# Kernel optimization log

Hardware: AMD Instinct MI355X
Metric: run time of the kernel (lower is better)

Reference implementation:

```python
import jax, jax.numpy as jnp
import numpy as np
from jax import lax

B, T, I, H, O = 128, 512, 256, 512, 256


def setup_inputs() -> dict:
    key = jax.random.key(0)
    ks = jax.random.split(key, 7)
    s_ih = 1.0 / np.sqrt(H)
    return {
        "inputs": jax.random.normal(ks[0], (B, T, I), dtype=jnp.float32),
        "W_ih": jax.random.uniform(ks[1], (H, I), jnp.float32, -s_ih, s_ih),
        "b_ih": jax.random.uniform(ks[2], (H,), jnp.float32, -s_ih, s_ih),
        "W_hh": jax.random.uniform(ks[3], (H, H), jnp.float32, -s_ih, s_ih),
        "b_hh": jax.random.uniform(ks[4], (H,), jnp.float32, -s_ih, s_ih),
        "W_out": jax.random.uniform(ks[5], (O, H), jnp.float32, -s_ih, s_ih),
        "b_out": jax.random.uniform(ks[6], (O,), jnp.float32, -s_ih, s_ih),
        "h0": jnp.zeros((H,), dtype=jnp.float32),
    }


def reference(inputs, W_ih, b_ih, W_hh, b_hh, W_out, b_out, h0):
    # inputs: [B, T, I]; returns readout of last hidden state: [B, O]
    Bsz, Tlen = inputs.shape[0], inputs.shape[1]
    inv_T = jnp.asarray(1.0 / Tlen, dtype=inputs.dtype)
    # Precompute input projection for all timesteps (one big GEMM):
    # x_proj[b,t,h] = inputs @ W_ih.T + b_ih + b_hh
    x_proj = jnp.einsum('bti,hi->bth', inputs, W_ih) + (b_ih + b_hh)
    x_proj_t = jnp.swapaxes(x_proj, 0, 1)  # [T, B, H]

    def step(h, xp):
        # RNNCell: tanh(xp + h @ W_hh.T); residual scaling by 1/T
        h_new = jnp.tanh(xp + h @ W_hh.T) * inv_T + h
        return h_new, None

    h_init = jnp.broadcast_to(h0, (Bsz, h0.shape[0]))
    h_last, _ = lax.scan(step, h_init, x_proj_t)
    return h_last @ W_out.T + b_out
```

## Files before the change

kernel.cpp:

```cpp
#include <hip/hip_runtime.h>
#include <stdint.h>

#define NB 128
#define NT 512
#define NI 256
#define NH 512
#define NO 256

__device__ __forceinline__ uint16_t f2bf(float x) {
  uint32_t u = __float_as_uint(x);
  return (uint16_t)((u + 0x7fffu + ((u >> 16) & 1u)) >> 16);
}
__device__ __forceinline__ uint32_t pack2bf(float a, float b) {
  return (uint32_t)f2bf(a) | ((uint32_t)f2bf(b) << 16);
}

__device__ __forceinline__ float fast_tanh(float x) {
  float e = __expf(2.0f * x);
#if __has_builtin(__builtin_amdgcn_rcpf)
  return 1.0f - 2.0f * __builtin_amdgcn_rcpf(e + 1.0f);
#else
  return 1.0f - 2.0f / (e + 1.0f);
#endif
}

typedef __bf16 bf16x8 __attribute__((ext_vector_type(8)));
typedef float f32x4 __attribute__((ext_vector_type(4)));

__device__ __forceinline__ f32x4 mfma16(bf16x8 a, uint4 b, f32x4 c) {
  return __builtin_amdgcn_mfma_f32_16x16x32_bf16(a, __builtin_bit_cast(bf16x8, b), c, 0, 0, 0);
}

__global__ __launch_bounds__(256) void prep_kernel(const float* __restrict__ Whh,
                                                   const float* __restrict__ Wih,
                                                   const float* __restrict__ Wout,
                                                   const float* __restrict__ bih,
                                                   const float* __restrict__ bhh,
                                                   uint4* __restrict__ WB,
                                                   float* __restrict__ WoT,
                                                   uint4* __restrict__ WihF,
                                                   float* __restrict__ BS) {
  int idx = blockIdx.x * 256 + threadIdx.x;
  if (idx < 32768) {
    int q = idx >> 9, t = idx & 511;
    int u = q >> 4, tk = q & 15;
    int n = (t >> 6) * 64 + u * 16 + (t & 15);
    int kb = tk * 32 + ((t >> 4) & 3) * 8;
    const float* row = Whh + (size_t)n * NH + kb;
    float4 f0 = *(const float4*)row;
    float4 f1 = *(const float4*)(row + 4);
    uint4 wq;
    wq.x = pack2bf(f0.x, f0.y);
    wq.y = pack2bf(f0.z, f0.w);
    wq.z = pack2bf(f1.x, f1.y);
    wq.w = pack2bf(f1.z, f1.w);
    WB[idx] = wq;
  } else if (idx < 49152) {
    int i = idx - 32768;
    int l = i & 63;
    int uk = i >> 6;
    int k0 = uk & 7, u = uk >> 3;
    int n = u * 16 + (l & 15);
    int kb = k0 * 32 + (l >> 4) * 8;
    const float* row = Wih + (size_t)n * NI + kb;
    float4 f0 = *(const float4*)row;
    float4 f1 = *(const float4*)(row + 4);
    uint4 wq;
    wq.x = pack2bf(f0.x, f0.y);
    wq.y = pack2bf(f0.z, f0.w);
    wq.z = pack2bf(f1.x, f1.y);
    wq.w = pack2bf(f1.z, f1.w);
    WihF[i] = wq;
  } else if (idx < 81920) {
    int i = idx - 49152;
    int o4 = (i & 63) * 4;
    int k = i >> 6;
    float4 v;
    v.x = Wout[(size_t)(o4 + 0) * NH + k];
    v.y = Wout[(size_t)(o4 + 1) * NH + k];
    v.z = Wout[(size_t)(o4 + 2) * NH + k];
    v.w = Wout[(size_t)(o4 + 3) * NH + k];
    *(float4*)&WoT[(size_t)k * NO + o4] = v;
  } else if (idx < 82432) {
    int n = idx - 81920;
    BS[n] = bih[n] + bhh[n];
  }
}

__global__ __launch_bounds__(256, 2) void xproj_kernel(const float* __restrict__ A,
                                                       const uint4* __restrict__ WihF,
                                                       const float* __restrict__ BS,
                                                       uint16_t* __restrict__ XP) {
  const int w = threadIdx.x >> 6;
  const int l = threadIdx.x & 63;
  const int sl = l & 15, quad = l >> 4;
  const int m = blockIdx.x * 64 + w * 16 + sl;

  f32x4 acc[32] = {};
  const float* arow = A + (size_t)m * NI;

  for (int k0 = 0; k0 < 8; ++k0) {
    float4 f0 = *(const float4*)(arow + k0 * 32 + quad * 8);
    float4 f1 = *(const float4*)(arow + k0 * 32 + quad * 8 + 4);
    uint4 ap;
    ap.x = pack2bf(f0.x, f0.y);
    ap.y = pack2bf(f0.z, f0.w);
    ap.z = pack2bf(f1.x, f1.y);
    ap.w = pack2bf(f1.z, f1.w);
    bf16x8 afrag = __builtin_bit_cast(bf16x8, ap);
#pragma unroll
    for (int u = 0; u < 32; ++u) {
      uint4 bp = WihF[(u * 8 + k0) * 64 + l];
      acc[u] = __builtin_amdgcn_mfma_f32_16x16x32_bf16(
          __builtin_bit_cast(bf16x8, bp), afrag, acc[u], 0, 0, 0);
    }
  }

  uint16_t* xrow = XP + (size_t)m * NH;
#pragma unroll
  for (int u = 0; u < 32; ++u) {
    float4 bs = *(const float4*)(BS + u * 16 + quad * 4);
    uint2 pw;
    pw.x = pack2bf(acc[u][0] + bs.x, acc[u][1] + bs.y);
    pw.y = pack2bf(acc[u][2] + bs.z, acc[u][3] + bs.w);
    *(uint2*)(xrow + u * 16 + quad * 4) = pw;
  }
}

__global__ __launch_bounds__(512, 2) void recur_kernel(const uint4* __restrict__ WB,
                                                       const float* __restrict__ WoT,
                                                       const uint16_t* __restrict__ XP,
                                                       const float* __restrict__ h0,
                                                       const float* __restrict__ bout,
                                                       float* __restrict__ out) {
  __shared__ uint4 WL[12][512];
  __shared__ __align__(16) uint16_t h2[2][NH];
  __shared__ float hsf[NH];
  const int t = threadIdx.x;
  const int b = blockIdx.x;
  const int w = t >> 6;
  const int sl = t & 15, quad = (t >> 4) & 3;
  const int myn = w * 64 + quad * 16 + sl;
  const float invT = 1.0f / (float)NT;

  uint4 Wr[52];
#pragma unroll
  for (int q = 0; q < 52; ++q) Wr[q] = WB[q * 512 + t];
#pragma unroll
  for (int i = 0; i < 12; ++i) WL[i][t] = WB[(52 + i) * 512 + t];

  float hj = h0[myn];
  h2[0][myn] = f2bf(hj);
  __syncthreads();

  const uint16_t* xpb = XP + (size_t)b * NT * NH + myn;

  for (int ts = 0; ts < NT; ++ts) {
    const int cur = ts & 1;
    float xpj = __uint_as_float((uint32_t)xpb[(size_t)ts * NH] << 16);

    const uint16_t* hbuf = h2[cur];
    f32x4 acc0 = {}, acc1 = {}, acc2 = {}, acc3 = {};
#pragma unroll
    for (int tk = 0; tk < 16; ++tk) {
      bf16x8 hfrag = *(const bf16x8*)(hbuf + tk * 32 + quad * 8);
      acc0 = mfma16(hfrag, Wr[tk], acc0);
      acc1 = mfma16(hfrag, Wr[16 + tk], acc1);
      acc2 = mfma16(hfrag, Wr[32 + tk], acc2);
      uint4 w3 = (tk < 4) ? Wr[48 + tk] : WL[tk - 4][t];
      acc3 = mfma16(hfrag, w3, acc3);
    }
    float y = (quad == 0) ? acc0[0] : (quad == 1) ? acc1[0] : (quad == 2) ? acc2[0] : acc3[0];
    float hnew = fmaf(fast_tanh(xpj + y), invT, hj);
    hj = hnew;
    h2[cur ^ 1][myn] = f2bf(hnew);
    __syncthreads();
  }

  hsf[myn] = hj;
  __syncthreads();

  if (t < NO) {
    float c0 = 0.f, c1 = 0.f;
#pragma unroll 4
    for (int k = 0; k < NH; k += 2) {
      c0 = fmaf(WoT[(size_t)k * NO + t], hsf[k], c0);
      c1 = fmaf(WoT[(size_t)(k + 1) * NO + t], hsf[k + 1], c1);
    }
    out[(size_t)b * NO + t] = c0 + c1 + bout[t];
  }
}

extern "C" void kernel_launch(void* const* d_in, const int* in_sizes, int n_in,
                              void* d_out, int out_size, void* d_ws, size_t ws_size,
                              hipStream_t stream) {
  const float* inputs = (const float*)d_in[0];
  const float* Wih    = (const float*)d_in[1];
  const float* bih    = (const float*)d_in[2];
  const float* Whh    = (const float*)d_in[3];
  const float* bhh    = (const float*)d_in[4];
  const float* Wout   = (const float*)d_in[5];
  const float* bout   = (const float*)d_in[6];
  const float* h0     = (const float*)d_in[7];
  float* out = (float*)d_out;

  char* ws = (char*)d_ws;
  uint4*    WB   = (uint4*)ws;
  float*    WoT  = (float*)(ws + (512u << 10));
  uint4*    WihF = (uint4*)(ws + (1024u << 10));
  float*    BS   = (float*)(ws + (1280u << 10));
  uint16_t* XP   = (uint16_t*)(ws + (1536u << 10));

  hipLaunchKernelGGL(prep_kernel, dim3(322), dim3(256), 0, stream,
                     Whh, Wih, Wout, bih, bhh, WB, WoT, WihF, BS);
  hipLaunchKernelGGL(xproj_kernel, dim3(NB * NT / 64), dim3(256), 0, stream,
                     inputs, WihF, BS, XP);
  hipLaunchKernelGGL(recur_kernel, dim3(NB), dim3(512), 0, stream,
                     WB, WoT, XP, h0, bout, out);
}
```

Measured before the change: 943.2 us.

## Retile input projection GEMM with register-resident weight slices and double-buffered A loads

The xproj kernel previously had each wave hold all 512 output columns for one 16-row tile and reload W_ih fragments from global memory for every MFMA. Now a 2D grid splits the N dimension into 8 groups of 64 columns. Each wave keeps its 32-fragment W_ih slice in registers, loops over 4 row tiles, and double-buffers the loading and bf16 packing of A rows to overlap them with the MFMAs. In exchange, the fp32 input rows are read 8 times, once per column group, instead of once, and register pressure from the resident weights remains.

```diff
diff --git a/kernel.cpp b/kernel.cpp
--- a/kernel.cpp
+++ b/kernel.cpp
@@ -29,6 +29,9 @@
 
 __device__ __forceinline__ f32x4 mfma16(bf16x8 a, uint4 b, f32x4 c) {
   return __builtin_amdgcn_mfma_f32_16x16x32_bf16(a, __builtin_bit_cast(bf16x8, b), c, 0, 0, 0);
+}
+__device__ __forceinline__ f32x4 mfma16_ab(uint4 a, bf16x8 b, f32x4 c) {
+  return __builtin_amdgcn_mfma_f32_16x16x32_bf16(__builtin_bit_cast(bf16x8, a), b, c, 0, 0, 0);
 }
 
 __global__ __launch_bounds__(256) void prep_kernel(const float* __restrict__ Whh,
@@ -87,6 +90,42 @@
   }
 }
 
+__device__ __forceinline__ void ld_pack(uint4 (&af)[8], const float* __restrict__ A,
+                                        int mt, int sl, int quad) {
+  const float* ar = A + (size_t)(mt * 16 + sl) * NI + quad * 8;
+#pragma unroll
+  for (int k0 = 0; k0 < 8; ++k0) {
+    float4 f0 = *(const float4*)(ar + k0 * 32);
+    float4 f1 = *(const float4*)(ar + k0 * 32 + 4);
+    uint4 ap;
+    ap.x = pack2bf(f0.x, f0.y);
+    ap.y = pack2bf(f0.z, f0.w);
+    ap.z = pack2bf(f1.x, f1.y);
+    ap.w = pack2bf(f1.z, f1.w);
+    af[k0] = ap;
+  }
+}
+
+__device__ __forceinline__ void do_tile(const uint4 (&af)[8], const uint4 (&Wb)[32],
+                                        const float4 (&bs)[4], uint16_t* __restrict__ XP,
+                                        int g, int mt, int sl, int quad) {
+  f32x4 acc[4] = {};
+#pragma unroll
+  for (int k0 = 0; k0 < 8; ++k0) {
+    bf16x8 a = __builtin_bit_cast(bf16x8, af[k0]);
+#pragma unroll
+    for (int u = 0; u < 4; ++u) acc[u] = mfma16_ab(Wb[u * 8 + k0], a, acc[u]);
+  }
+  uint16_t* xrow = XP + (size_t)(mt * 16 + sl) * NH + g * 64 + quad * 4;
+#pragma unroll
+  for (int u = 0; u < 4; ++u) {
+    uint2 pw;
+    pw.x = pack2bf(acc[u][0] + bs[u].x, acc[u][1] + bs[u].y);
+    pw.y = pack2bf(acc[u][2] + bs[u].z, acc[u][3] + bs[u].w);
+    *(uint2*)(xrow + u * 16) = pw;
+  }
+}
+
 __global__ __launch_bounds__(256, 2) void xproj_kernel(const float* __restrict__ A,
                                                        const uint4* __restrict__ WihF,
                                                        const float* __restrict__ BS,
@@ -94,37 +133,29 @@
   const int w = threadIdx.x >> 6;
   const int l = threadIdx.x & 63;
   const int sl = l & 15, quad = l >> 4;
-  const int m = blockIdx.x * 64 + w * 16 + sl;
-
-  f32x4 acc[32] = {};
-  const float* arow = A + (size_t)m * NI;
-
-  for (int k0 = 0; k0 < 8; ++k0) {
-    float4 f0 = *(const float4*)(arow + k0 * 32 + quad * 8);
-    float4 f1 = *(const float4*)(arow + k0 * 32 + quad * 8 + 4);
-    uint4 ap;
-    ap.x = pack2bf(f0.x, f0.y);
-    ap.y = pack2bf(f0.z, f0.w);
-    ap.z = pack2bf(f1.x, f1.y);
-    ap.w = pack2bf(f1.z, f1.w);
-    bf16x8 afrag = __builtin_bit_cast(bf16x8, ap);
-#pragma unroll
-    for (int u = 0; u < 32; ++u) {
-      uint4 bp = WihF[(u * 8 + k0) * 64 + l];
-      acc[u] = __builtin_amdgcn_mfma_f32_16x16x32_bf16(
-          __builtin_bit_cast(bf16x8, bp), afrag, acc[u], 0, 0, 0);
-    }
-  }
-
-  uint16_t* xrow = XP + (size_t)m * NH;
-#pragma unroll
-  for (int u = 0; u < 32; ++u) {
-    float4 bs = *(const float4*)(BS + u * 16 + quad * 4);
-    uint2 pw;
-    pw.x = pack2bf(acc[u][0] + bs.x, acc[u][1] + bs.y);
-    pw.y = pack2bf(acc[u][2] + bs.z, acc[u][3] + bs.w);
-    *(uint2*)(xrow + u * 16 + quad * 4) = pw;
-  }
+  const int g = blockIdx.y;
+  const int mt0 = blockIdx.x * 16 + w * 4;
+
+  uint4 Wb[32];
+#pragma unroll
+  for (int u = 0; u < 4; ++u)
+#pragma unroll
+    for (int k0 = 0; k0 < 8; ++k0)
+      Wb[u * 8 + k0] = WihF[(size_t)((g * 4 + u) * 8 + k0) * 64 + l];
+
+  float4 bs[4];
+#pragma unroll
+  for (int u = 0; u < 4; ++u) bs[u] = *(const float4*)(BS + (g * 4 + u) * 16 + quad * 4);
+
+  uint4 afA[8], afB[8];
+  ld_pack(afA, A, mt0 + 0, sl, quad);
+  ld_pack(afB, A, mt0 + 1, sl, quad);
+  do_tile(afA, Wb, bs, XP, g, mt0 + 0, sl, quad);
+  ld_pack(afA, A, mt0 + 2, sl, quad);
+  do_tile(afB, Wb, bs, XP, g, mt0 + 1, sl, quad);
+  ld_pack(afB, A, mt0 + 3, sl, quad);
+  do_tile(afA, Wb, bs, XP, g, mt0 + 2, sl, quad);
+  do_tile(afB, Wb, bs, XP, g, mt0 + 3, sl, quad);
 }
 
 __global__ __launch_bounds__(512, 2) void recur_kernel(const uint4* __restrict__ WB,
@@ -213,7 +244,7 @@
 
   hipLaunchKernelGGL(prep_kernel, dim3(322), dim3(256), 0, stream,
                      Whh, Wih, Wout, bih, bhh, WB, WoT, WihF, BS);
-  hipLaunchKernelGGL(xproj_kernel, dim3(NB * NT / 64), dim3(256), 0, stream,
+  hipLaunchKernelGGL(xproj_kernel, dim3(NB * NT / 256, 8), dim3(256), 0, stream,
                      inputs, WihF, BS, XP);
   hipLaunchKernelGGL(recur_kernel, dim3(NB), dim3(512), 0, stream,
                      WB, WoT, XP, h0, bout, out);
```

Measured after the change: 929.9 us. Within noise of the previous version (-1.4%).

## Keep W_ih fragments in registers in xproj and stage A tiles via LDS

Applied to the files above, without the earlier changes.

The input-projection kernel now has each wave hold its 128-column slice of W_ih in registers for the whole block. Each block loops over 16 row tiles, converting input rows to bf16 into double-buffered shared memory. This removes the repeated global loads of W_ih for every 64-row tile and reuses the weights across 256 rows, at the cost of 64 uint4 registers per thread and fewer blocks. The recurrence kernel also keeps all 64 W_hh fragments in registers instead of spilling 12 into LDS, which raises register pressure and risks spills or lower occupancy.

```diff
diff --git a/kernel.cpp b/kernel.cpp
--- a/kernel.cpp
+++ b/kernel.cpp
@@ -29,6 +29,9 @@
 
 __device__ __forceinline__ f32x4 mfma16(bf16x8 a, uint4 b, f32x4 c) {
   return __builtin_amdgcn_mfma_f32_16x16x32_bf16(a, __builtin_bit_cast(bf16x8, b), c, 0, 0, 0);
+}
+__device__ __forceinline__ f32x4 mfma16_ab(uint4 a, bf16x8 b, f32x4 c) {
+  return __builtin_amdgcn_mfma_f32_16x16x32_bf16(__builtin_bit_cast(bf16x8, a), b, c, 0, 0, 0);
 }
 
 __global__ __launch_bounds__(256) void prep_kernel(const float* __restrict__ Whh,
@@ -87,43 +90,82 @@
   }
 }
 
-__global__ __launch_bounds__(256, 2) void xproj_kernel(const float* __restrict__ A,
-                                                       const uint4* __restrict__ WihF,
-                                                       const float* __restrict__ BS,
-                                                       uint16_t* __restrict__ XP) {
-  const int w = threadIdx.x >> 6;
-  const int l = threadIdx.x & 63;
+#define XMT 16
+#define AROW 528
+__global__ __launch_bounds__(256) void xproj_kernel(const float* __restrict__ A,
+                                                    const uint4* __restrict__ WihF,
+                                                    const float* __restrict__ BS,
+                                                    uint16_t* __restrict__ XP) {
+  __shared__ __align__(16) uint8_t Asm[2][16 * AROW];
+  const int tid = threadIdx.x;
+  const int w = tid >> 6;
+  const int l = tid & 63;
   const int sl = l & 15, quad = l >> 4;
-  const int m = blockIdx.x * 64 + w * 16 + sl;
-
-  f32x4 acc[32] = {};
-  const float* arow = A + (size_t)m * NI;
-
-  for (int k0 = 0; k0 < 8; ++k0) {
-    float4 f0 = *(const float4*)(arow + k0 * 32 + quad * 8);
-    float4 f1 = *(const float4*)(arow + k0 * 32 + quad * 8 + 4);
-    uint4 ap;
-    ap.x = pack2bf(f0.x, f0.y);
-    ap.y = pack2bf(f0.z, f0.w);
-    ap.z = pack2bf(f1.x, f1.y);
-    ap.w = pack2bf(f1.z, f1.w);
-    bf16x8 afrag = __builtin_bit_cast(bf16x8, ap);
-#pragma unroll
-    for (int u = 0; u < 32; ++u) {
-      uint4 bp = WihF[(u * 8 + k0) * 64 + l];
-      acc[u] = __builtin_amdgcn_mfma_f32_16x16x32_bf16(
-          __builtin_bit_cast(bf16x8, bp), afrag, acc[u], 0, 0, 0);
-    }
-  }
-
-  uint16_t* xrow = XP + (size_t)m * NH;
-#pragma unroll
-  for (int u = 0; u < 32; ++u) {
-    float4 bs = *(const float4*)(BS + u * 16 + quad * 4);
-    uint2 pw;
-    pw.x = pack2bf(acc[u][0] + bs.x, acc[u][1] + bs.y);
-    pw.y = pack2bf(acc[u][2] + bs.z, acc[u][3] + bs.w);
-    *(uint2*)(xrow + u * 16 + quad * 4) = pw;
+  const int mt0 = blockIdx.x * XMT;
+  const int srow = tid >> 4;
+  const int sseg = tid & 15;
+
+  uint4 Wb[64];
+#pragma unroll
+  for (int u8 = 0; u8 < 8; ++u8)
+#pragma unroll
+    for (int k0 = 0; k0 < 8; ++k0)
+      Wb[u8 * 8 + k0] = WihF[(size_t)((w * 8 + u8) * 8 + k0) * 64 + l];
+
+  float4 bs[8];
+#pragma unroll
+  for (int u8 = 0; u8 < 8; ++u8)
+    bs[u8] = *(const float4*)(BS + (w * 8 + u8) * 16 + quad * 4);
+
+  {
+    const float* ar = A + (size_t)(mt0 * 16 + srow) * NI + sseg * 16;
+    float4 f0 = *(const float4*)ar, f1 = *(const float4*)(ar + 4);
+    float4 f2 = *(const float4*)(ar + 8), f3 = *(const float4*)(ar + 12);
+    uint4 p0, p1;
+    p0.x = pack2bf(f0.x, f0.y); p0.y = pack2bf(f0.z, f0.w);
+    p0.z = pack2bf(f1.x, f1.y); p0.w = pack2bf(f1.z, f1.w);
+    p1.x = pack2bf(f2.x, f2.y); p1.y = pack2bf(f2.z, f2.w);
+    p1.z = pack2bf(f3.x, f3.y); p1.w = pack2bf(f3.z, f3.w);
+    uint8_t* dst = &Asm[0][srow * AROW + sseg * 32];
+    *(uint4*)dst = p0;
+    *(uint4*)(dst + 16) = p1;
+  }
+  __syncthreads();
+
+  for (int i = 0; i < XMT; ++i) {
+    const int bb = i & 1;
+    if (i + 1 < XMT) {
+      const float* ar = A + (size_t)((mt0 + i + 1) * 16 + srow) * NI + sseg * 16;
+      float4 f0 = *(const float4*)ar, f1 = *(const float4*)(ar + 4);
+      float4 f2 = *(const float4*)(ar + 8), f3 = *(const float4*)(ar + 12);
+      uint4 p0, p1;
+      p0.x = pack2bf(f0.x, f0.y); p0.y = pack2bf(f0.z, f0.w);
+      p0.z = pack2bf(f1.x, f1.y); p0.w = pack2bf(f1.z, f1.w);
+      p1.x = pack2bf(f2.x, f2.y); p1.y = pack2bf(f2.z, f2.w);
+      p1.z = pack2bf(f3.x, f3.y); p1.w = pack2bf(f3.z, f3.w);
+      uint8_t* dst = &Asm[bb ^ 1][srow * AROW + sseg * 32];
+      *(uint4*)dst = p0;
+      *(uint4*)(dst + 16) = p1;
+    }
+
+    f32x4 acc[8] = {};
+    const uint8_t* abase = &Asm[bb][sl * AROW + quad * 16];
+#pragma unroll
+    for (int k0 = 0; k0 < 8; ++k0) {
+      bf16x8 a = *(const bf16x8*)(abase + k0 * 64);
+#pragma unroll
+      for (int u8 = 0; u8 < 8; ++u8)
+        acc[u8] = mfma16_ab(Wb[u8 * 8 + k0], a, acc[u8]);
+    }
+    uint16_t* xrow = XP + (size_t)((mt0 + i) * 16 + sl) * NH + w * 128 + quad * 4;
+#pragma unroll
+    for (int u8 = 0; u8 < 8; ++u8) {
+      uint2 pw;
+      pw.x = pack2bf(acc[u8][0] + bs[u8].x, acc[u8][1] + bs[u8].y);
+      pw.y = pack2bf(acc[u8][2] + bs[u8].z, acc[u8][3] + bs[u8].w);
+      *(uint2*)(xrow + u8 * 16) = pw;
+    }
+    __syncthreads();
   }
 }
 
@@ -133,7 +175,6 @@
                                                        const float* __restrict__ h0,
                                                        const float* __restrict__ bout,
                                                        float* __restrict__ out) {
-  __shared__ uint4 WL[12][512];
   __shared__ __align__(16) uint16_t h2[2][NH];
   __shared__ float hsf[NH];
   const int t = threadIdx.x;
@@ -143,11 +184,9 @@
   const int myn = w * 64 + quad * 16 + sl;
   const float invT = 1.0f / (float)NT;
 
-  uint4 Wr[52];
-#pragma unroll
-  for (int q = 0; q < 52; ++q) Wr[q] = WB[q * 512 + t];
-#pragma unroll
-  for (int i = 0; i < 12; ++i) WL[i][t] = WB[(52 + i) * 512 + t];
+  uint4 Wr[64];
+#pragma unroll
+  for (int q = 0; q < 64; ++q) Wr[q] = WB[q * 512 + t];
 
   float hj = h0[myn];
   h2[0][myn] = f2bf(hj);
@@ -167,8 +206,7 @@
       acc0 = mfma16(hfrag, Wr[tk], acc0);
       acc1 = mfma16(hfrag, Wr[16 + tk], acc1);
       acc2 = mfma16(hfrag, Wr[32 + tk], acc2);
-      uint4 w3 = (tk < 4) ? Wr[48 + tk] : WL[tk - 4][t];
-      acc3 = mfma16(hfrag, w3, acc3);
+      acc3 = mfma16(hfrag, Wr[48 + tk], acc3);
     }
     float y = (quad == 0) ? acc0[0] : (quad == 1) ? acc1[0] : (quad == 2) ? acc2[0] : acc3[0];
     float hnew = fmaf(fast_tanh(xpj + y), invT, hj);
@@ -213,7 +251,7 @@
 
   hipLaunchKernelGGL(prep_kernel, dim3(322), dim3(256), 0, stream,
                      Whh, Wih, Wout, bih, bhh, WB, WoT, WihF, BS);
-  hipLaunchKernelGGL(xproj_kernel, dim3(NB * NT / 64), dim3(256), 0, stream,
+  hipLaunchKernelGGL(xproj_kernel, dim3(NB * NT / (XMT * 16)), dim3(256), 0, stream,
                      inputs, WihF, BS, XP);
   hipLaunchKernelGGL(recur_kernel, dim3(NB), dim3(512), 0, stream,
                      WB, WoT, XP, h0, bout, out);
```

Result: slower. 1.570 ms (+66.4%).
